# Optimization experiments

Hardware: AMD Instinct MI355X
Metric: run time of the kernel (lower is better)

## Reference

```python
import jax, jax.numpy as jnp
import numpy as np

B, L, HID = 16, 512, 768
HEADS, M = 12, 4
EMB, BLK, NER, NCLS = 768, 8, 6, 97


def setup_inputs() -> dict:
    key = jax.random.key(0)
    ks = jax.random.split(key, 10)
    return {
        "sequence_output": jax.random.normal(ks[0], (B, L, HID), jnp.float32),
        "attention": jax.random.uniform(ks[1], (B, HEADS, L, L), jnp.float32),
        "entity_pos": jax.random.randint(ks[2], (B, 2, M), 0, L - 2),
        "hs_ner_tags": jax.random.uniform(ks[3], (B, NER), jnp.float32),
        "ts_ner_tags": jax.random.uniform(ks[4], (B, NER), jnp.float32),
        "Wh": jax.random.normal(ks[5], (EMB, 2 * HID + NER), jnp.float32) * 0.02,
        "bh": jnp.zeros((EMB,), jnp.float32),
        "Wt": jax.random.normal(ks[6], (EMB, 2 * HID + NER), jnp.float32) * 0.02,
        "bt": jnp.zeros((EMB,), jnp.float32),
        "Wb": jax.random.normal(ks[7], (NCLS, EMB * BLK), jnp.float32) * 0.02,
        "bb": jnp.zeros((NCLS,), jnp.float32),
    }


def reference(sequence_output, attention, entity_pos, hs_ner_tags, ts_ner_tags,
              Wh, bh, Wt, bt, Wb, bb):
    b_idx = jnp.arange(B)[:, None, None]            # [B,1,1]
    starts = entity_pos + 1                         # [B,2,M] (all < L by construction)

    # entity embeddings: gather mention token embeddings, logsumexp-pool over mentions
    ment_emb = sequence_output[b_idx, starts]       # [B,2,M,HID]
    ent_emb = jax.scipy.special.logsumexp(ment_emb, axis=2)  # [B,2,HID]

    # entity attentions: gather mention attention rows, mean-pool over mentions
    attn_t = attention.transpose(0, 2, 1, 3)        # [B,L,HEADS,L]
    ment_att = attn_t[b_idx, starts]                # [B,2,M,HEADS,L]
    ent_att = ment_att.mean(axis=2)                 # [B,2,HEADS,L]

    hs, ts = ent_emb[:, 0], ent_emb[:, 1]           # [B,HID]
    h_att, t_att = ent_att[:, 0], ent_att[:, 1]     # [B,HEADS,L]

    ht_att = (h_att * t_att).mean(axis=1)           # [B,L]
    ht_att = ht_att / (ht_att.sum(axis=1, keepdims=True) + 1e-5)
    rs = jnp.einsum('bld,bl->bd', sequence_output, ht_att)  # [B,HID]

    hs2 = jnp.tanh(jnp.concatenate([hs, rs, hs_ner_tags], axis=1) @ Wh.T + bh)
    ts2 = jnp.tanh(jnp.concatenate([ts, rs, ts_ner_tags], axis=1) @ Wt.T + bt)

    b1 = hs2.reshape(B, EMB // BLK, BLK)
    b2 = ts2.reshape(B, EMB // BLK, BLK)
    bl = (b1[:, :, :, None] * b2[:, :, None, :]).reshape(B, EMB * BLK)
    logits = bl @ Wb.T + bb                         # [B, NCLS]
    return logits
```

## Files before the change

### kernel.cpp

```cpp
#include <hip/hip_runtime.h>
#include <math.h>

#define B 16
#define L 512
#define HID 768
#define HEADS 12
#define M 4
#define EMB 768
#define BLK 8
#define NER 6
#define NCLS 97
#define CAT (2*HID + NER)
#define EB (EMB*BLK)
#define NCH 8
#define CATP 1544

__global__ void k_front(const float* __restrict__ seq, const float* __restrict__ att,
                        const int* __restrict__ epos,
                        float* __restrict__ ent, float* __restrict__ ht) {
    int b = blockIdx.x;
    __shared__ int ss[2][M];
    if (threadIdx.x < 2*M) {
        int e = threadIdx.x >> 2, m = threadIdx.x & 3;
        ss[e][m] = epos[(b*2+e)*M + m] + 1;
    }
    __syncthreads();

    int l = threadIdx.x;
    float raw = 0.f;
    for (int h = 0; h < HEADS; ++h) {
        const float* ah = att + ((size_t)b*HEADS + h)*L*L;
        float a0 = 0.f, a1 = 0.f;
        #pragma unroll
        for (int m = 0; m < M; ++m) {
            a0 += ah[(size_t)ss[0][m]*L + l];
            a1 += ah[(size_t)ss[1][m]*L + l];
        }
        raw += a0*a1;
    }
    raw *= (1.f/(M*M*HEADS));
    float v = raw;
    for (int off = 32; off; off >>= 1) v += __shfl_down(v, off);
    __shared__ float wsum[8];
    __shared__ float tot;
    int wid = threadIdx.x >> 6, lane = threadIdx.x & 63;
    if (lane == 0) wsum[wid] = v;
    __syncthreads();
    if (threadIdx.x == 0) {
        float t = 0.f;
        #pragma unroll
        for (int i = 0; i < 8; ++i) t += wsum[i];
        tot = t + 1e-5f;
    }
    __syncthreads();
    ht[b*L + l] = raw / tot;

    const float* base = seq + (size_t)b*L*HID;
    for (int idx = threadIdx.x; idx < 2*HID; idx += 512) {
        int e = (idx >= HID) ? 1 : 0;
        int d = idx - e*HID;
        float v0 = base[(size_t)ss[e][0]*HID + d];
        float v1 = base[(size_t)ss[e][1]*HID + d];
        float v2 = base[(size_t)ss[e][2]*HID + d];
        float v3 = base[(size_t)ss[e][3]*HID + d];
        float mx = fmaxf(fmaxf(v0, v1), fmaxf(v2, v3));
        float s = expf(v0-mx) + expf(v1-mx) + expf(v2-mx) + expf(v3-mx);
        ent[((size_t)e*B + b)*HID + d] = mx + logf(s);
    }
}

__global__ void k_rs_part(const float* __restrict__ seq, const float* __restrict__ ht,
                          float* __restrict__ part) {
    int b = blockIdx.x, ch = blockIdx.y;
    const int LC = L/NCH;
    __shared__ float hl[L/NCH];
    if (threadIdx.x < LC) hl[threadIdx.x] = ht[b*L + ch*LC + threadIdx.x];
    __syncthreads();
    const float4* sp = (const float4*)(seq + (size_t)b*L*HID + (size_t)ch*LC*HID);
    float4 acc = make_float4(0.f, 0.f, 0.f, 0.f);
    for (int i = 0; i < LC; ++i) {
        float4 vv = sp[i*(HID/4) + threadIdx.x];
        float w = hl[i];
        acc.x += vv.x*w; acc.y += vv.y*w; acc.z += vv.z*w; acc.w += vv.w*w;
    }
    ((float4*)(part + ((size_t)ch*B + b)*HID))[threadIdx.x] = acc;
}

__launch_bounds__(512)
__global__ void k_proj(const float* __restrict__ Wh, const float* __restrict__ bh,
                       const float* __restrict__ Wt, const float* __restrict__ bt,
                       const float* __restrict__ ent, const float* __restrict__ part,
                       const float* __restrict__ hner, const float* __restrict__ tner,
                       float* __restrict__ out) {
    int t = blockIdx.y, zh = blockIdx.z;
    __shared__ float act[8*CATP];
    const float* e0  = ent + (size_t)t*B*HID;
    const float* ner = t ? tner : hner;
    for (int bi = 0; bi < 8; ++bi) {
        int gb = zh*8 + bi;
        for (int k = threadIdx.x; k < CAT; k += 512) {
            float v;
            if (k < HID) {
                v = e0[gb*HID + k];
            } else if (k < 2*HID) {
                int kk = k - HID;
                float s = 0.f;
                #pragma unroll
                for (int c = 0; c < NCH; ++c) s += part[((size_t)c*B + gb)*HID + kk];
                v = s;
            } else {
                v = ner[gb*NER + (k - 2*HID)];
            }
            act[bi*CATP + k] = v;
        }
    }
    __syncthreads();

    int wid = threadIdx.x >> 6, lane = threadIdx.x & 63;
    int j = blockIdx.x*8 + wid;
    const float* wrow = (t ? Wt : Wh) + (size_t)j*CAT;
    float acc[8];
    #pragma unroll
    for (int b = 0; b < 8; ++b) acc[b] = 0.f;
    for (int i = 0; i < 25; ++i) {
        int k = i*64 + lane;
        if (k < CAT) {
            float w = wrow[k];
            #pragma unroll
            for (int b = 0; b < 8; ++b) acc[b] += w * act[b*CATP + k];
        }
    }
    for (int off = 32; off; off >>= 1)
        #pragma unroll
        for (int b = 0; b < 8; ++b) acc[b] += __shfl_down(acc[b], off);
    if (lane == 0) {
        float bj = (t ? bt : bh)[j];
        #pragma unroll
        for (int b = 0; b < 8; ++b)
            out[((size_t)t*B + zh*8 + b)*EMB + j] = tanhf(acc[b] + bj);
    }
}

__launch_bounds__(512)
__global__ void k_logits(const float* __restrict__ Wb, const float* __restrict__ bb,
                         const float* __restrict__ proj, float* __restrict__ out) {
    int c = blockIdx.x;
    const float* wr = Wb + (size_t)c*EB;
    const float* ph = proj;
    const float* pt = proj + (size_t)B*EMB;
    float acc[B];
    #pragma unroll
    for (int b = 0; b < B; ++b) acc[b] = 0.f;
    for (int k = threadIdx.x; k < EB; k += 512) {
        int g = k >> 6, r = (k >> 3) & 7, cc = k & 7;
        float w = wr[k];
        int o = g*8;
        #pragma unroll
        for (int b = 0; b < B; ++b)
            acc[b] += w * ph[b*EMB + o + r] * pt[b*EMB + o + cc];
    }
    int wid = threadIdx.x >> 6, lane = threadIdx.x & 63;
    for (int off = 32; off; off >>= 1)
        #pragma unroll
        for (int b = 0; b < B; ++b) acc[b] += __shfl_down(acc[b], off);
    __shared__ float partl[8][B];
    if (lane == 0)
        #pragma unroll
        for (int b = 0; b < B; ++b) partl[wid][b] = acc[b];
    __syncthreads();
    if (threadIdx.x < B) {
        int b = threadIdx.x;
        float s = 0.f;
        #pragma unroll
        for (int w = 0; w < 8; ++w) s += partl[w][b];
        out[b*NCLS + c] = s + bb[c];
    }
}

extern "C" void kernel_launch(void* const* d_in, const int* in_sizes, int n_in,
                              void* d_out, int out_size, void* d_ws, size_t ws_size,
                              hipStream_t stream) {
    const float* seq  = (const float*)d_in[0];
    const float* att  = (const float*)d_in[1];
    const int*   epos = (const int*)  d_in[2];
    const float* hner = (const float*)d_in[3];
    const float* tner = (const float*)d_in[4];
    const float* Wh   = (const float*)d_in[5];
    const float* bh   = (const float*)d_in[6];
    const float* Wt   = (const float*)d_in[7];
    const float* bt   = (const float*)d_in[8];
    const float* Wb   = (const float*)d_in[9];
    const float* bb   = (const float*)d_in[10];
    float* out = (float*)d_out;

    float* ws   = (float*)d_ws;
    float* ent  = ws;
    float* ht   = ent  + 2*B*HID;
    float* part = ht   + B*L;
    float* proj = part + (size_t)NCH*B*HID;

    k_front  <<<dim3(B),          512, 0, stream>>>(seq, att, epos, ent, ht);
    k_rs_part<<<dim3(B, NCH),     192, 0, stream>>>(seq, ht, part);
    k_proj   <<<dim3(EMB/8, 2, 2),512, 0, stream>>>(Wh, bh, Wt, bt, ent, part, hner, tner, proj);
    k_logits <<<dim3(NCLS),       512, 0, stream>>>(Wb, bb, proj, out);
}
```

Measured before the change: 338.3 us.

## Split attention pooling across heads, atomic rs reduction, materialize bilinear features

```diff
diff --git a/kernel.cpp b/kernel.cpp
--- a/kernel.cpp
+++ b/kernel.cpp
@@ -13,12 +13,12 @@
 #define CAT (2*HID + NER)
 #define EB (EMB*BLK)
 #define NCH 8
-#define CATP 1544
-
-__global__ void k_front(const float* __restrict__ seq, const float* __restrict__ att,
-                        const int* __restrict__ epos,
-                        float* __restrict__ ent, float* __restrict__ ht) {
-    int b = blockIdx.x;
+
+__global__ void k_att(const float* __restrict__ att, const float* __restrict__ seq,
+                      const int* __restrict__ epos,
+                      float* __restrict__ pp, float* __restrict__ ent,
+                      float* __restrict__ rs) {
+    int b = blockIdx.x, h = blockIdx.y;
     __shared__ int ss[2][M];
     if (threadIdx.x < 2*M) {
         int e = threadIdx.x >> 2, m = threadIdx.x & 3;
@@ -27,92 +27,88 @@
     __syncthreads();
 
     int l = threadIdx.x;
-    float raw = 0.f;
-    for (int h = 0; h < HEADS; ++h) {
-        const float* ah = att + ((size_t)b*HEADS + h)*L*L;
-        float a0 = 0.f, a1 = 0.f;
-        #pragma unroll
-        for (int m = 0; m < M; ++m) {
-            a0 += ah[(size_t)ss[0][m]*L + l];
-            a1 += ah[(size_t)ss[1][m]*L + l];
+    const float* ah = att + ((size_t)b*HEADS + h)*L*L;
+    float a0 = 0.f, a1 = 0.f;
+    #pragma unroll
+    for (int m = 0; m < M; ++m) {
+        a0 += ah[(size_t)ss[0][m]*L + l];
+        a1 += ah[(size_t)ss[1][m]*L + l];
+    }
+    pp[((size_t)b*HEADS + h)*L + l] = a0*a1;
+
+    if (h < 2) {
+        const float* base = seq + (size_t)b*L*HID;
+        for (int d = threadIdx.x; d < HID; d += 512) {
+            float v0 = base[(size_t)ss[h][0]*HID + d];
+            float v1 = base[(size_t)ss[h][1]*HID + d];
+            float v2 = base[(size_t)ss[h][2]*HID + d];
+            float v3 = base[(size_t)ss[h][3]*HID + d];
+            float mx = fmaxf(fmaxf(v0, v1), fmaxf(v2, v3));
+            float s = expf(v0-mx) + expf(v1-mx) + expf(v2-mx) + expf(v3-mx);
+            ent[((size_t)h*B + b)*HID + d] = mx + logf(s);
         }
-        raw += a0*a1;
-    }
-    raw *= (1.f/(M*M*HEADS));
-    float v = raw;
-    for (int off = 32; off; off >>= 1) v += __shfl_down(v, off);
-    __shared__ float wsum[8];
-    __shared__ float tot;
+    } else if (h == 2) {
+        for (int d = threadIdx.x; d < HID; d += 512) rs[b*HID + d] = 0.f;
+    }
+}
+
+__launch_bounds__(192)
+__global__ void k_rs(const float* __restrict__ seq, const float* __restrict__ pp,
+                     float* __restrict__ rs) {
+    int b = blockIdx.x, ch = blockIdx.y;
+    __shared__ float sraw[L];
+    __shared__ float red[3];
+    __shared__ float sinv;
+    float psum = 0.f;
+    for (int l = threadIdx.x; l < L; l += 192) {
+        float r = 0.f;
+        #pragma unroll
+        for (int h = 0; h < HEADS; ++h) r += pp[((size_t)b*HEADS + h)*L + l];
+        r *= (1.f/(M*M*HEADS));
+        sraw[l] = r;
+        psum += r;
+    }
+    for (int off = 32; off; off >>= 1) psum += __shfl_down(psum, off);
     int wid = threadIdx.x >> 6, lane = threadIdx.x & 63;
-    if (lane == 0) wsum[wid] = v;
-    __syncthreads();
-    if (threadIdx.x == 0) {
-        float t = 0.f;
-        #pragma unroll
-        for (int i = 0; i < 8; ++i) t += wsum[i];
-        tot = t + 1e-5f;
-    }
-    __syncthreads();
-    ht[b*L + l] = raw / tot;
-
-    const float* base = seq + (size_t)b*L*HID;
-    for (int idx = threadIdx.x; idx < 2*HID; idx += 512) {
-        int e = (idx >= HID) ? 1 : 0;
-        int d = idx - e*HID;
-        float v0 = base[(size_t)ss[e][0]*HID + d];
-        float v1 = base[(size_t)ss[e][1]*HID + d];
-        float v2 = base[(size_t)ss[e][2]*HID + d];
-        float v3 = base[(size_t)ss[e][3]*HID + d];
-        float mx = fmaxf(fmaxf(v0, v1), fmaxf(v2, v3));
-        float s = expf(v0-mx) + expf(v1-mx) + expf(v2-mx) + expf(v3-mx);
-        ent[((size_t)e*B + b)*HID + d] = mx + logf(s);
-    }
-}
-
-__global__ void k_rs_part(const float* __restrict__ seq, const float* __restrict__ ht,
-                          float* __restrict__ part) {
-    int b = blockIdx.x, ch = blockIdx.y;
-    const int LC = L/NCH;
-    __shared__ float hl[L/NCH];
-    if (threadIdx.x < LC) hl[threadIdx.x] = ht[b*L + ch*LC + threadIdx.x];
-    __syncthreads();
-    const float4* sp = (const float4*)(seq + (size_t)b*L*HID + (size_t)ch*LC*HID);
+    if (lane == 0) red[wid] = psum;
+    __syncthreads();
+    if (threadIdx.x == 0) sinv = 1.f/(red[0] + red[1] + red[2] + 1e-5f);
+    __syncthreads();
+    float inv = sinv;
+
+    const float4* sp = (const float4*)(seq + (size_t)b*L*HID + (size_t)ch*(L/NCH)*HID);
     float4 acc = make_float4(0.f, 0.f, 0.f, 0.f);
-    for (int i = 0; i < LC; ++i) {
-        float4 vv = sp[i*(HID/4) + threadIdx.x];
-        float w = hl[i];
-        acc.x += vv.x*w; acc.y += vv.y*w; acc.z += vv.z*w; acc.w += vv.w*w;
-    }
-    ((float4*)(part + ((size_t)ch*B + b)*HID))[threadIdx.x] = acc;
+    for (int i = 0; i < L/NCH; ++i) {
+        float w = sraw[ch*(L/NCH) + i] * inv;
+        float4 v = sp[i*(HID/4) + threadIdx.x];
+        acc.x += v.x*w; acc.y += v.y*w; acc.z += v.z*w; acc.w += v.w*w;
+    }
+    float* rp = rs + b*HID + threadIdx.x*4;
+    atomicAdd(rp+0, acc.x);
+    atomicAdd(rp+1, acc.y);
+    atomicAdd(rp+2, acc.z);
+    atomicAdd(rp+3, acc.w);
 }
 
 __launch_bounds__(512)
 __global__ void k_proj(const float* __restrict__ Wh, const float* __restrict__ bh,
                        const float* __restrict__ Wt, const float* __restrict__ bt,
-                       const float* __restrict__ ent, const float* __restrict__ part,
+                       const float* __restrict__ ent, const float* __restrict__ rs,
                        const float* __restrict__ hner, const float* __restrict__ tner,
                        float* __restrict__ out) {
     int t = blockIdx.y, zh = blockIdx.z;
-    __shared__ float act[8*CATP];
+    __shared__ float actA[CAT*4];
+    __shared__ float actB[CAT*4];
     const float* e0  = ent + (size_t)t*B*HID;
     const float* ner = t ? tner : hner;
-    for (int bi = 0; bi < 8; ++bi) {
+    for (int idx = threadIdx.x; idx < CAT*8; idx += 512) {
+        int k = idx >> 3, bi = idx & 7;
         int gb = zh*8 + bi;
-        for (int k = threadIdx.x; k < CAT; k += 512) {
-            float v;
-            if (k < HID) {
-                v = e0[gb*HID + k];
-            } else if (k < 2*HID) {
-                int kk = k - HID;
-                float s = 0.f;
-                #pragma unroll
-                for (int c = 0; c < NCH; ++c) s += part[((size_t)c*B + gb)*HID + kk];
-                v = s;
-            } else {
-                v = ner[gb*NER + (k - 2*HID)];
-            }
-            act[bi*CATP + k] = v;
-        }
+        float v;
+        if (k < HID)            v = e0[gb*HID + k];
+        else if (k < 2*HID)     v = rs[gb*HID + (k - HID)];
+        else                    v = ner[gb*NER + (k - 2*HID)];
+        if (bi < 4) actA[k*4 + bi] = v; else actB[k*4 + bi - 4] = v;
     }
     __syncthreads();
 
@@ -126,8 +122,10 @@
         int k = i*64 + lane;
         if (k < CAT) {
             float w = wrow[k];
-            #pragma unroll
-            for (int b = 0; b < 8; ++b) acc[b] += w * act[b*CATP + k];
+            float4 a = *(const float4*)&actA[k*4];
+            float4 c = *(const float4*)&actB[k*4];
+            acc[0] += w*a.x; acc[1] += w*a.y; acc[2] += w*a.z; acc[3] += w*a.w;
+            acc[4] += w*c.x; acc[5] += w*c.y; acc[6] += w*c.z; acc[7] += w*c.w;
         }
     }
     for (int off = 32; off; off >>= 1)
@@ -141,23 +139,35 @@
     }
 }
 
+__global__ void k_bl(const float* __restrict__ proj, float* __restrict__ bl) {
+    int b = blockIdx.x;
+    const float* ph = proj + (size_t)b*EMB;
+    const float* pt = proj + (size_t)B*EMB + (size_t)b*EMB;
+    for (int i4 = threadIdx.x; i4 < EB/4; i4 += 512) {
+        int k = i4*4;
+        int g = k >> 6, r = (k >> 3) & 7, c0 = k & 7;
+        float pr = ph[g*8 + r];
+        float4 q = *(const float4*)(pt + g*8 + c0);
+        float4 o = make_float4(pr*q.x, pr*q.y, pr*q.z, pr*q.w);
+        ((float4*)(bl + (size_t)b*EB))[i4] = o;
+    }
+}
+
 __launch_bounds__(512)
 __global__ void k_logits(const float* __restrict__ Wb, const float* __restrict__ bb,
-                         const float* __restrict__ proj, float* __restrict__ out) {
+                         const float* __restrict__ bl, float* __restrict__ out) {
     int c = blockIdx.x;
-    const float* wr = Wb + (size_t)c*EB;
-    const float* ph = proj;
-    const float* pt = proj + (size_t)B*EMB;
+    const float4* wr = (const float4*)(Wb + (size_t)c*EB);
     float acc[B];
     #pragma unroll
     for (int b = 0; b < B; ++b) acc[b] = 0.f;
-    for (int k = threadIdx.x; k < EB; k += 512) {
-        int g = k >> 6, r = (k >> 3) & 7, cc = k & 7;
-        float w = wr[k];
-        int o = g*8;
-        #pragma unroll
-        for (int b = 0; b < B; ++b)
-            acc[b] += w * ph[b*EMB + o + r] * pt[b*EMB + o + cc];
+    for (int i = threadIdx.x; i < EB/4; i += 512) {
+        float4 w = wr[i];
+        #pragma unroll
+        for (int b = 0; b < B; ++b) {
+            float4 v = ((const float4*)(bl + (size_t)b*EB))[i];
+            acc[b] += w.x*v.x + w.y*v.y + w.z*v.z + w.w*v.w;
+        }
     }
     int wid = threadIdx.x >> 6, lane = threadIdx.x & 63;
     for (int off = 32; off; off >>= 1)
@@ -194,13 +204,15 @@
     float* out = (float*)d_out;
 
     float* ws   = (float*)d_ws;
-    float* ent  = ws;
-    float* ht   = ent  + 2*B*HID;
-    float* part = ht   + B*L;
-    float* proj = part + (size_t)NCH*B*HID;
-
-    k_front  <<<dim3(B),          512, 0, stream>>>(seq, att, epos, ent, ht);
-    k_rs_part<<<dim3(B, NCH),     192, 0, stream>>>(seq, ht, part);
-    k_proj   <<<dim3(EMB/8, 2, 2),512, 0, stream>>>(Wh, bh, Wt, bt, ent, part, hner, tner, proj);
-    k_logits <<<dim3(NCLS),       512, 0, stream>>>(Wb, bb, proj, out);
-}
+    float* pp   = ws;
+    float* ent  = pp   + (size_t)B*HEADS*L;
+    float* rs   = ent  + 2*B*HID;
+    float* proj = rs   + B*HID;
+    float* bl   = proj + 2*B*EMB;
+
+    k_att   <<<dim3(B, HEADS), 512, 0, stream>>>(att, seq, epos, pp, ent, rs);
+    k_rs    <<<dim3(B, NCH),   192, 0, stream>>>(seq, pp, rs);
+    k_proj  <<<dim3(EMB/8, 2, 2), 512, 0, stream>>>(Wh, bh, Wt, bt, ent, rs, hner, tner, proj);
+    k_bl    <<<dim3(B),        512, 0, stream>>>(proj, bl);
+    k_logits<<<dim3(NCLS),     512, 0, stream>>>(Wb, bb, bl, out);
+}
```

New measurement: 295.7 us. 12.6% less time.
